# Kernel tuning notes

Measured on AMD Instinct MI355X. Metric: run time of the kernel, lower is better.

## Reference

```python
import jax, jax.numpy as jnp
import numpy as np

SR = 10  # self.sr in the torch module

def _linear_params(key, fan_in, fan_out):
    kw, kb = jax.random.split(key)
    bound = 1.0 / np.sqrt(fan_in)
    W = jax.random.uniform(kw, (fan_out, fan_in), jnp.float32, -bound, bound)
    b = jax.random.uniform(kb, (fan_out,), jnp.float32, -bound, bound)
    return W, b

def setup_inputs() -> dict:
    key = jax.random.key(0)
    ks = jax.random.split(key, 6)
    P, H = 2048, 1024
    R = C = P * SR
    X = jax.random.normal(ks[0], (R, C), jnp.float32)
    p = jax.random.randint(ks[1], (P,), 0, 64, jnp.int32)
    W1, b1 = _linear_params(ks[2], 1, H)
    W2, b2 = _linear_params(ks[3], H, H)
    W3, b3 = _linear_params(ks[4], H, H)
    W4, b4 = _linear_params(ks[5], H, 1)
    return {"X": X, "p": p, "W1": W1, "b1": b1, "W2": W2, "b2": b2,
            "W3": W3, "b3": b3, "W4": W4, "b4": b4}

def _forward(X, p, W1, b1, W2, b2, W3, b3, W4, b4):
    P = p.shape[0]
    C = X.shape[1]
    # shift_rows: only rows i*SR for i in [0, P-2] are populated; all other
    # rows of the shifted matrix are NaN and contribute 0 sum / 0 count below.
    rows = X[jnp.arange(P - 1) * SR]                      # (P-1, C)
    shifts = p[: P - 1]
    # torch.roll(x, s): out[j] = x[(j - s) mod C]
    cols = (jnp.arange(C)[None, :] - shifts[:, None]) % C  # (P-1, C)
    shifted = jnp.take_along_axis(rows, cols, axis=1)      # (P-1, C)
    # nan_mean over rows (NaN rows of the full matrix drop out identically)
    mask = jnp.isnan(shifted)
    col_sum = jnp.where(mask, 0.0, shifted).sum(axis=0)
    col_cnt = (~mask).sum(axis=0).astype(jnp.float32)
    m = jnp.where(col_cnt > 0, col_sum / col_cnt, jnp.float32(jnp.nan))  # (C,)
    # fill_nan_with_last_value: serial forward-fill (index 0 kept as-is)
    def step(last, xi):
        v = jnp.where(jnp.isnan(xi), last, xi)
        return v, v
    _, rest = jax.lax.scan(step, m[0], m[1:])
    filled = jnp.concatenate([m[:1], rest])                # (C,)
    x = filled[::SR][:P][:, None]                          # (P, 1)
    h = jax.nn.relu(x @ W1.T + b1)
    h = jax.nn.relu(h @ W2.T + b2)
    h = jax.nn.relu(h @ W3.T + b3)
    y = h @ W4.T + b4                                      # (P, 1)
    return y[:, 0]

def reference(X, p, W1, b1, W2, b2, W3, b3, W4, b4):
    return _forward(X, p, W1, b1, W2, b2, W3, b3, W4, b4)
```

## Files before the change

kernel.cpp:

```cpp
#include <hip/hip_runtime.h>
#include <hip/hip_bf16.h>

#define CC 20480
#define PP 2048
#define NROWS 2047
#define SRR 10
#define HH 1024
#define NCH 64

typedef __attribute__((ext_vector_type(8))) short short8;
typedef __attribute__((ext_vector_type(4))) float f32x4;

__device__ __forceinline__ void split_bf16(float v, unsigned short& hi, unsigned short& lo) {
    __hip_bfloat16 h = __float2bfloat16(v);
    float r = v - __bfloat162float(h);
    __hip_bfloat16 l2 = __float2bfloat16(r);
    hi = *(unsigned short*)&h;
    lo = *(unsigned short*)&l2;
}

__global__ __launch_bounds__(256) void pre_k(const float* __restrict__ X,
                                             const int* __restrict__ p,
                                             float* __restrict__ psum,
                                             const float* __restrict__ W2,
                                             unsigned short* __restrict__ w2h,
                                             unsigned short* __restrict__ w2l,
                                             const float* __restrict__ W3,
                                             unsigned short* __restrict__ w3h,
                                             unsigned short* __restrict__ w3l) {
    int b = blockIdx.x, t = threadIdx.x;
    if (b < 512) {
        int k = (b & 7) * 256 + t;
        int chunk = b >> 3;
        int r0 = chunk * 32;
        int r1 = r0 + 32; if (r1 > NROWS) r1 = NROWS;
        float s = 0.f;
        int base = SRR * k;
        for (int i = r0; i < r1; ++i) {
            int col = base - p[i]; if (col < 0) col += CC;
            s += X[(size_t)i * (size_t)(SRR * CC) + col];
        }
        psum[chunk * PP + k] = s;
        return;
    }
    int bb = b - 512;
    const float* src; unsigned short *dh, *dl;
    if (bb < 256) { src = W2; dh = w2h; dl = w2l; }
    else { src = W3; dh = w3h; dl = w3l; bb -= 256; }
    int idx = bb * 4096 + t * 16;
    #pragma unroll
    for (int q = 0; q < 4; ++q) {
        float4 v = *(const float4*)&src[idx + q * 4];
        float vv[4] = {v.x, v.y, v.z, v.w};
        ushort hi4[4], lo4[4];
        #pragma unroll
        for (int i = 0; i < 4; ++i) split_bf16(vv[i], hi4[i], lo4[i]);
        *(ushort4*)&dh[idx + q * 4] = *(ushort4*)hi4;
        *(ushort4*)&dl[idx + q * 4] = *(ushort4*)lo4;
    }
}

__device__ __forceinline__ void gload16(const unsigned short* g, unsigned short* lds) {
    __builtin_amdgcn_global_load_lds(
        (const __attribute__((address_space(1))) void*)g,
        (__attribute__((address_space(3))) void*)lds,
        16, 0, 0);
}

#define BM 128
#define BN 64
#define BK 32

__global__ __launch_bounds__(512, 2) void gemm1_k(
    const float* __restrict__ psum,
    const float* __restrict__ W1, const float* __restrict__ b1,
    const unsigned short* __restrict__ Bh, const unsigned short* __restrict__ Bl,
    const float* __restrict__ b2,
    unsigned short* __restrict__ Ch, unsigned short* __restrict__ Cl)
{
    __shared__ unsigned short Bb[3][4096];
    __shared__ float w1f[1024], b1f[1024], xv[128];

    int lin = blockIdx.x;
    int v = (lin & 7) * 32 + (lin >> 3);
    int bx = v >> 4, by = v & 15;
    int bm = bx * BM, bn = by * BN;
    int t = threadIdx.x, w = t >> 6, l = t & 63;
    int lr = l & 15, lk = l >> 4;
    int wr = w >> 1, wc = w & 1;

    size_t offB = (size_t)(bn + (w & 3) * 16 + lr) * HH + lk * 8;
#define BSTAGE(buf, k0)                                                      \
    do {                                                                     \
        if (w < 4) gload16(Bh + offB + (k0), Bb[buf] + w * 512);             \
        else       gload16(Bl + offB + (k0), Bb[buf] + 2048 + (w - 4) * 512);\
    } while (0)

    BSTAGE(0, 0);
    {
        int row = t >> 2, q = t & 3;
        float s = 0.f;
        #pragma unroll
        for (int j = 0; j < 16; ++j) s += psum[(q * 16 + j) * PP + bm + row];
        s += __shfl_xor(s, 1, 64);
        s += __shfl_xor(s, 2, 64);
        if (q == 0) xv[row] = s * (1.0f / (float)NROWS);
        if (t < 256) *(float4*)&w1f[t * 4] = *(const float4*)&W1[t * 4];
        else *(float4*)&b1f[(t - 256) * 4] = *(const float4*)&b1[(t - 256) * 4];
    }
    __syncthreads();

    float x0 = xv[wr * 32 + lr], x1 = xv[wr * 32 + 16 + lr];

    f32x4 acc[2][2];
    #pragma unroll
    for (int i = 0; i < 2; ++i)
        #pragma unroll
        for (int j = 0; j < 2; ++j) acc[i][j] = (f32x4)(0.f);

    int nt = HH / BK;
    for (int tt = 0; tt < nt; ++tt) {
        int cur = tt % 3;
        if (tt + 1 < nt) {
            BSTAGE((tt + 1) % 3, (tt + 1) * BK);
            asm volatile("s_waitcnt vmcnt(1)" ::: "memory");
        } else {
            asm volatile("s_waitcnt vmcnt(0)" ::: "memory");
        }
        __builtin_amdgcn_s_barrier();
        __builtin_amdgcn_sched_barrier(0);
        __builtin_amdgcn_s_setprio(1);
        int k0 = tt * BK;
        float4 wva = *(const float4*)&w1f[k0 + lk * 8];
        float4 wvb = *(const float4*)&w1f[k0 + lk * 8 + 4];
        float4 bva = *(const float4*)&b1f[k0 + lk * 8];
        float4 bvb = *(const float4*)&b1f[k0 + lk * 8 + 4];
        float wv[8] = {wva.x, wva.y, wva.z, wva.w, wvb.x, wvb.y, wvb.z, wvb.w};
        float bv2[8] = {bva.x, bva.y, bva.z, bva.w, bvb.x, bvb.y, bvb.z, bvb.w};
        ushort ahh[2][8], all2[2][8];
        #pragma unroll
        for (int mi = 0; mi < 2; ++mi) {
            float xm = mi ? x1 : x0;
            #pragma unroll
            for (int j = 0; j < 8; ++j) {
                float h = fmaf(xm, wv[j], bv2[j]);
                h = h > 0.f ? h : 0.f;
                split_bf16(h, ahh[mi][j], all2[mi][j]);
            }
        }
        short8 bh2[2], bl2[2];
        #pragma unroll
        for (int ni = 0; ni < 2; ++ni) {
            bh2[ni] = *(const short8*)&Bb[cur][(wc * 2 + ni) * 512 + l * 8];
            bl2[ni] = *(const short8*)&Bb[cur][2048 + (wc * 2 + ni) * 512 + l * 8];
        }
        #pragma unroll
        for (int mi = 0; mi < 2; ++mi) {
            short8 ah2 = *(short8*)ahh[mi];
            short8 al2 = *(short8*)all2[mi];
            #pragma unroll
            for (int ni = 0; ni < 2; ++ni) {
                acc[mi][ni] = __builtin_amdgcn_mfma_f32_16x16x32_bf16(ah2, bh2[ni], acc[mi][ni], 0, 0, 0);
                acc[mi][ni] = __builtin_amdgcn_mfma_f32_16x16x32_bf16(ah2, bl2[ni], acc[mi][ni], 0, 0, 0);
                acc[mi][ni] = __builtin_amdgcn_mfma_f32_16x16x32_bf16(al2, bh2[ni], acc[mi][ni], 0, 0, 0);
            }
        }
        __builtin_amdgcn_s_setprio(0);
        __builtin_amdgcn_sched_barrier(0);
    }
#undef BSTAGE

    float bv[2];
    #pragma unroll
    for (int ni = 0; ni < 2; ++ni) bv[ni] = b2[bn + wc * 32 + ni * 16 + lr];
    #pragma unroll
    for (int mi = 0; mi < 2; ++mi)
        #pragma unroll
        for (int ni = 0; ni < 2; ++ni)
            #pragma unroll
            for (int r = 0; r < 4; ++r) {
                int row = bm + wr * 32 + mi * 16 + lk * 4 + r;
                int col = bn + wc * 32 + ni * 16 + lr;
                float vv = acc[mi][ni][r] + bv[ni];
                vv = vv > 0.f ? vv : 0.f;
                unsigned short hi, lo;
                split_bf16(vv, hi, lo);
                Ch[(size_t)row * HH + col] = hi;
                Cl[(size_t)row * HH + col] = lo;
            }
}

__global__ __launch_bounds__(512, 2) void gemm2_k(
    const unsigned short* __restrict__ Ah, const unsigned short* __restrict__ Al,
    const unsigned short* __restrict__ Bh, const unsigned short* __restrict__ Bl,
    const float* __restrict__ b3,
    const float* __restrict__ W4, float* __restrict__ partial)
{
    __shared__ unsigned short lds[3][12288];
    int lin = blockIdx.x;
    int v = (lin & 7) * 32 + (lin >> 3);
    int bx = v >> 4, by = v & 15;
    int bm = bx * BM, bn = by * BN;
    int t = threadIdx.x, w = t >> 6, l = t & 63;
    int lr = l & 15, lk = l >> 4;
    int wr = w >> 1, wc = w & 1;

    size_t offA = (size_t)(bm + w * 16 + lr) * HH + lk * 8;
    size_t offB = (size_t)(bn + (w & 3) * 16 + lr) * HH + lk * 8;

#define STAGE(buf, k0)                                                   \
    do {                                                                 \
        unsigned short* L = lds[buf];                                    \
        gload16(Ah + offA + (k0), L + w * 512);                          \
        gload16(Al + offA + (k0), L + 4096 + w * 512);                   \
        if (w < 4) gload16(Bh + offB + (k0), L + 8192 + w * 512);        \
        else       gload16(Bl + offB + (k0), L + 10240 + (w - 4) * 512); \
    } while (0)

    f32x4 acc[2][2];
    #pragma unroll
    for (int i = 0; i < 2; ++i)
        #pragma unroll
        for (int j = 0; j < 2; ++j) acc[i][j] = (f32x4)(0.f);

    STAGE(0, 0);

    int nt = HH / BK;
    for (int tt = 0; tt < nt; ++tt) {
        int cur = tt % 3;
        if (tt + 1 < nt) {
            STAGE((tt + 1) % 3, (tt + 1) * BK);
            asm volatile("s_waitcnt vmcnt(3)" ::: "memory");
        } else {
            asm volatile("s_waitcnt vmcnt(0)" ::: "memory");
        }
        __builtin_amdgcn_s_barrier();
        __builtin_amdgcn_sched_barrier(0);
        __builtin_amdgcn_s_setprio(1);
        unsigned short* L = lds[cur];
        short8 ah2[2], al2[2], bh2[2], bl2[2];
        #pragma unroll
        for (int mi = 0; mi < 2; ++mi) {
            ah2[mi] = *(const short8*)&L[(wr * 2 + mi) * 512 + l * 8];
            al2[mi] = *(const short8*)&L[4096 + (wr * 2 + mi) * 512 + l * 8];
        }
        #pragma unroll
        for (int ni = 0; ni < 2; ++ni) {
            bh2[ni] = *(const short8*)&L[8192 + (wc * 2 + ni) * 512 + l * 8];
            bl2[ni] = *(const short8*)&L[10240 + (wc * 2 + ni) * 512 + l * 8];
        }
        #pragma unroll
        for (int mi = 0; mi < 2; ++mi)
            #pragma unroll
            for (int ni = 0; ni < 2; ++ni) {
                acc[mi][ni] = __builtin_amdgcn_mfma_f32_16x16x32_bf16(ah2[mi], bh2[ni], acc[mi][ni], 0, 0, 0);
                acc[mi][ni] = __builtin_amdgcn_mfma_f32_16x16x32_bf16(ah2[mi], bl2[ni], acc[mi][ni], 0, 0, 0);
                acc[mi][ni] = __builtin_amdgcn_mfma_f32_16x16x32_bf16(al2[mi], bh2[ni], acc[mi][ni], 0, 0, 0);
            }
        __builtin_amdgcn_s_setprio(0);
        __builtin_amdgcn_sched_barrier(0);
    }
#undef STAGE

    float bv[2], w4v[2];
    #pragma unroll
    for (int ni = 0; ni < 2; ++ni) {
        bv[ni]  = b3[bn + wc * 32 + ni * 16 + lr];
        w4v[ni] = W4[bn + wc * 32 + ni * 16 + lr];
    }
    #pragma unroll
    for (int mi = 0; mi < 2; ++mi) {
        float ps[4];
        #pragma unroll
        for (int r = 0; r < 4; ++r) {
            float acc_d = 0.f;
            #pragma unroll
            for (int ni = 0; ni < 2; ++ni) {
                float vv = acc[mi][ni][r] + bv[ni];
                vv = vv > 0.f ? vv : 0.f;
                acc_d += vv * w4v[ni];
            }
            ps[r] = acc_d;
        }
        #pragma unroll
        for (int r = 0; r < 4; ++r) {
            #pragma unroll
            for (int m2 = 1; m2 < 16; m2 <<= 1) ps[r] += __shfl_xor(ps[r], m2, 64);
        }
        if (lr == 0) {
            #pragma unroll
            for (int r = 0; r < 4; ++r) {
                int row = bm + wr * 32 + mi * 16 + lk * 4 + r;
                partial[(size_t)row * 32 + by * 2 + wc] = ps[r];
            }
        }
    }
}

__global__ __launch_bounds__(256) void ysum_k(const float* __restrict__ partial,
                                              const float* __restrict__ b4,
                                              float* __restrict__ y) {
    int r = blockIdx.x * 256 + threadIdx.x;
    float s = 0.f;
    #pragma unroll
    for (int q = 0; q < 8; ++q) {
        float4 v = *(const float4*)&partial[(size_t)r * 32 + q * 4];
        s += v.x + v.y + v.z + v.w;
    }
    y[r] = s + b4[0];
}

extern "C" void kernel_launch(void* const* d_in, const int* in_sizes, int n_in,
                              void* d_out, int out_size, void* d_ws, size_t ws_size,
                              hipStream_t stream) {
    const float* X  = (const float*)d_in[0];
    const int*   p  = (const int*)d_in[1];
    const float* W1 = (const float*)d_in[2];
    const float* b1 = (const float*)d_in[3];
    const float* W2 = (const float*)d_in[4];
    const float* b2 = (const float*)d_in[5];
    const float* W3 = (const float*)d_in[6];
    const float* b3 = (const float*)d_in[7];
    const float* W4 = (const float*)d_in[8];
    const float* b4 = (const float*)d_in[9];
    float* out = (float*)d_out;

    char* ws = (char*)d_ws;
    size_t off = 0;
    float* psum = (float*)(ws + off); off += (size_t)NCH * PP * 4;
    unsigned short* h2h = (unsigned short*)(ws + off); off += (size_t)PP * HH * 2;
    unsigned short* h2l = (unsigned short*)(ws + off); off += (size_t)PP * HH * 2;
    unsigned short* w2h = (unsigned short*)(ws + off); off += (size_t)HH * HH * 2;
    unsigned short* w2l = (unsigned short*)(ws + off); off += (size_t)HH * HH * 2;
    unsigned short* w3h = (unsigned short*)(ws + off); off += (size_t)HH * HH * 2;
    unsigned short* w3l = (unsigned short*)(ws + off); off += (size_t)HH * HH * 2;
    float* partial = (float*)(ws + off); off += (size_t)PP * 32 * 4;

    pre_k<<<1024, 256, 0, stream>>>(X, p, psum, W2, w2h, w2l, W3, w3h, w3l);
    gemm1_k<<<256, 512, 0, stream>>>(psum, W1, b1, w2h, w2l, b2, h2h, h2l);
    gemm2_k<<<256, 512, 0, stream>>>(h2h, h2l, w3h, w3l, b3, W4, partial);
    ysum_k<<<PP / 256, 256, 0, stream>>>(partial, b4, out);
}
```

Measured before the change: 81.88 us.

## Replace first hidden GEMM with piecewise-linear breakpoint tables over scalar input

Because the MLP input is a scalar x, layer-2 pre-activations are piecewise linear in x with breakpoints at -b1/W1. The change sorts the breakpoints, builds prefix-sum slope/intercept tables (Atab/Ctab) with a scan kernel over transposed W2, then evaluates h2 per row by binary search and one FMA per output. This removes the 2048x1024x1024 split-bf16 GEMM and is exact in fp32, at the cost of a serial 256-step scan kernel, a bitonic sort in one block, strided transpose writes, and 8 MB of tables.

Measured after the change: 145.1 us. +77.2%, slower.

```diff
diff --git a/kernel.cpp b/kernel.cpp
--- a/kernel.cpp
+++ b/kernel.cpp
@@ -23,11 +23,18 @@
                                              const int* __restrict__ p,
                                              float* __restrict__ psum,
                                              const float* __restrict__ W2,
-                                             unsigned short* __restrict__ w2h,
-                                             unsigned short* __restrict__ w2l,
+                                             float* __restrict__ w2t,
                                              const float* __restrict__ W3,
                                              unsigned short* __restrict__ w3h,
-                                             unsigned short* __restrict__ w3l) {
+                                             unsigned short* __restrict__ w3l,
+                                             const float* __restrict__ W1,
+                                             const float* __restrict__ b1,
+                                             float* __restrict__ tsort,
+                                             int* __restrict__ ord,
+                                             float* __restrict__ cA,
+                                             float* __restrict__ cC,
+                                             float* __restrict__ cI,
+                                             float* __restrict__ cIC) {
     int b = blockIdx.x, t = threadIdx.x;
     if (b < 512) {
         int k = (b & 7) * 256 + t;
@@ -43,20 +50,156 @@
         psum[chunk * PP + k] = s;
         return;
     }
-    int bb = b - 512;
-    const float* src; unsigned short *dh, *dl;
-    if (bb < 256) { src = W2; dh = w2h; dl = w2l; }
-    else { src = W3; dh = w3h; dl = w3l; bb -= 256; }
-    int idx = bb * 4096 + t * 16;
-    #pragma unroll
-    for (int q = 0; q < 4; ++q) {
-        float4 v = *(const float4*)&src[idx + q * 4];
-        float vv[4] = {v.x, v.y, v.z, v.w};
-        ushort hi4[4], lo4[4];
-        #pragma unroll
-        for (int i = 0; i < 4; ++i) split_bf16(vv[i], hi4[i], lo4[i]);
-        *(ushort4*)&dh[idx + q * 4] = *(ushort4*)hi4;
-        *(ushort4*)&dl[idx + q * 4] = *(ushort4*)lo4;
+    if (b < 768) {
+        int bb = b - 512;
+        int idx = bb * 4096 + t * 16;
+        int n2 = idx >> 10;
+        int o0 = idx & 1023;
+        #pragma unroll
+        for (int q = 0; q < 4; ++q) {
+            float4 v = *(const float4*)&W2[idx + q * 4];
+            w2t[(size_t)(o0 + q * 4 + 0) * 1024 + n2] = v.x;
+            w2t[(size_t)(o0 + q * 4 + 1) * 1024 + n2] = v.y;
+            w2t[(size_t)(o0 + q * 4 + 2) * 1024 + n2] = v.z;
+            w2t[(size_t)(o0 + q * 4 + 3) * 1024 + n2] = v.w;
+        }
+        return;
+    }
+    if (b < 1024) {
+        int bb = b - 768;
+        int idx = bb * 4096 + t * 16;
+        #pragma unroll
+        for (int q = 0; q < 4; ++q) {
+            float4 v = *(const float4*)&W3[idx + q * 4];
+            float vv[4] = {v.x, v.y, v.z, v.w};
+            ushort hi4[4], lo4[4];
+            #pragma unroll
+            for (int i = 0; i < 4; ++i) split_bf16(vv[i], hi4[i], lo4[i]);
+            *(ushort4*)&w3h[idx + q * 4] = *(ushort4*)hi4;
+            *(ushort4*)&w3l[idx + q * 4] = *(ushort4*)lo4;
+        }
+        return;
+    }
+    __shared__ float ks[1024];
+    __shared__ int vs[1024];
+    const float PINF = __int_as_float(0x7f800000);
+    for (int i = t; i < 1024; i += 256) {
+        float w1 = W1[i], bv = b1[i];
+        float tv;
+        if (w1 != 0.f) tv = -bv / w1;
+        else tv = (bv > 0.f) ? -PINF : PINF;
+        ks[i] = tv; vs[i] = i;
+    }
+    __syncthreads();
+    for (int size = 2; size <= 1024; size <<= 1)
+        for (int stride = size >> 1; stride; stride >>= 1) {
+            for (int i = t; i < 1024; i += 256) {
+                int jx = i ^ stride;
+                if (jx > i) {
+                    bool up = ((i & size) == 0);
+                    float a = ks[i], bq = ks[jx];
+                    bool sw = up ? (a > bq) : (a < bq);
+                    if (sw) {
+                        ks[i] = bq; ks[jx] = a;
+                        int tmp = vs[i]; vs[i] = vs[jx]; vs[jx] = tmp;
+                    }
+                }
+            }
+            __syncthreads();
+        }
+    for (int i = t; i < 1024; i += 256) {
+        int o = vs[i];
+        float w1 = W1[o], bv = b1[o];
+        float s = (w1 < 0.f) ? -1.f : 1.f;
+        tsort[i] = ks[i]; ord[i] = o;
+        cA[i] = s * w1;  cC[i] = s * bv;
+        cI[i] = (w1 < 0.f) ? w1 : 0.f;
+        cIC[i] = (w1 < 0.f) ? bv : 0.f;
+    }
+}
+
+__global__ __launch_bounds__(256) void scan_k(const float* __restrict__ w2t,
+                                              const int* __restrict__ ord,
+                                              const float* __restrict__ cA,
+                                              const float* __restrict__ cC,
+                                              const float* __restrict__ cI,
+                                              const float* __restrict__ cIC,
+                                              float* __restrict__ Atab,
+                                              float* __restrict__ Ctab,
+                                              const float* __restrict__ psum,
+                                              float* __restrict__ xbuf) {
+    int b = blockIdx.x, t = threadIdx.x;
+    if (b >= 16) {
+        int k = (b - 16) * 256 + t;
+        float s = 0.f;
+        #pragma unroll 8
+        for (int c = 0; c < NCH; ++c) s += psum[c * PP + k];
+        xbuf[k] = s * (1.0f / (float)NROWS);
+        return;
+    }
+    __shared__ float sA[4][64], sC[4][64], sIA[4][64], sIC[4][64];
+    int q = t >> 6, n = t & 63;
+    int n2 = b * 64 + n;
+    float gA = 0.f, gC = 0.f, iA = 0.f, iC = 0.f;
+    #pragma unroll 4
+    for (int step = 0; step < 256; ++step) {
+        int j = q * 256 + step;
+        int o = ord[j];
+        float wv = w2t[(size_t)o * 1024 + n2];
+        gA = fmaf(cA[j], wv, gA);
+        gC = fmaf(cC[j], wv, gC);
+        iA = fmaf(cI[j], wv, iA);
+        iC = fmaf(cIC[j], wv, iC);
+    }
+    sA[q][n] = gA; sC[q][n] = gC; sIA[q][n] = iA; sIC[q][n] = iC;
+    __syncthreads();
+    float offA = sIA[0][n] + sIA[1][n] + sIA[2][n] + sIA[3][n];
+    float offC = sIC[0][n] + sIC[1][n] + sIC[2][n] + sIC[3][n];
+    #pragma unroll
+    for (int q2 = 0; q2 < 4; ++q2)
+        if (q2 < q) { offA += sA[q2][n]; offC += sC[q2][n]; }
+    if (q == 0) { Atab[n2] = offA; Ctab[n2] = offC; }
+    float g2 = offA, h2 = offC;
+    #pragma unroll 4
+    for (int step = 0; step < 256; ++step) {
+        int j = q * 256 + step;
+        int o = ord[j];
+        float wv = w2t[(size_t)o * 1024 + n2];
+        g2 = fmaf(cA[j], wv, g2);
+        h2 = fmaf(cC[j], wv, h2);
+        Atab[(size_t)(j + 1) * 1024 + n2] = g2;
+        Ctab[(size_t)(j + 1) * 1024 + n2] = h2;
+    }
+}
+
+__global__ __launch_bounds__(512) void evalh2_k(const float* __restrict__ tsort,
+                                                const float* __restrict__ Atab,
+                                                const float* __restrict__ Ctab,
+                                                const float* __restrict__ b2,
+                                                const float* __restrict__ xbuf,
+                                                unsigned short* __restrict__ h2h,
+                                                unsigned short* __restrict__ h2l) {
+    __shared__ float ts[1024];
+    int t = threadIdx.x;
+    for (int i = t; i < 1024; i += 512) ts[i] = tsort[i];
+    __syncthreads();
+    int wv = t >> 6, lane = t & 63;
+    int k = blockIdx.x * 8 + wv;
+    float x = xbuf[k];
+    int lo = 0, hi = 1024;
+    while (lo < hi) { int mid = (lo + hi) >> 1; if (ts[mid] < x) lo = mid + 1; else hi = mid; }
+    const float* Ac = Atab + (size_t)lo * 1024;
+    const float* Cc = Ctab + (size_t)lo * 1024;
+    #pragma unroll
+    for (int s2 = 0; s2 < 16; ++s2) {
+        int n2 = s2 * 64 + lane;
+        float a = Ac[n2], c = Cc[n2], bb = b2[n2];
+        float h = fmaf(a, x, c + bb);
+        h = h > 0.f ? h : 0.f;
+        unsigned short hh, hl;
+        split_bf16(h, hh, hl);
+        h2h[(size_t)k * 1024 + n2] = hh;
+        h2l[(size_t)k * 1024 + n2] = hl;
     }
 }
 
@@ -70,125 +213,6 @@
 #define BM 128
 #define BN 64
 #define BK 32
-
-__global__ __launch_bounds__(512, 2) void gemm1_k(
-    const float* __restrict__ psum,
-    const float* __restrict__ W1, const float* __restrict__ b1,
-    const unsigned short* __restrict__ Bh, const unsigned short* __restrict__ Bl,
-    const float* __restrict__ b2,
-    unsigned short* __restrict__ Ch, unsigned short* __restrict__ Cl)
-{
-    __shared__ unsigned short Bb[3][4096];
-    __shared__ float w1f[1024], b1f[1024], xv[128];
-
-    int lin = blockIdx.x;
-    int v = (lin & 7) * 32 + (lin >> 3);
-    int bx = v >> 4, by = v & 15;
-    int bm = bx * BM, bn = by * BN;
-    int t = threadIdx.x, w = t >> 6, l = t & 63;
-    int lr = l & 15, lk = l >> 4;
-    int wr = w >> 1, wc = w & 1;
-
-    size_t offB = (size_t)(bn + (w & 3) * 16 + lr) * HH + lk * 8;
-#define BSTAGE(buf, k0)                                                      \
-    do {                                                                     \
-        if (w < 4) gload16(Bh + offB + (k0), Bb[buf] + w * 512);             \
-        else       gload16(Bl + offB + (k0), Bb[buf] + 2048 + (w - 4) * 512);\
-    } while (0)
-
-    BSTAGE(0, 0);
-    {
-        int row = t >> 2, q = t & 3;
-        float s = 0.f;
-        #pragma unroll
-        for (int j = 0; j < 16; ++j) s += psum[(q * 16 + j) * PP + bm + row];
-        s += __shfl_xor(s, 1, 64);
-        s += __shfl_xor(s, 2, 64);
-        if (q == 0) xv[row] = s * (1.0f / (float)NROWS);
-        if (t < 256) *(float4*)&w1f[t * 4] = *(const float4*)&W1[t * 4];
-        else *(float4*)&b1f[(t - 256) * 4] = *(const float4*)&b1[(t - 256) * 4];
-    }
-    __syncthreads();
-
-    float x0 = xv[wr * 32 + lr], x1 = xv[wr * 32 + 16 + lr];
-
-    f32x4 acc[2][2];
-    #pragma unroll
-    for (int i = 0; i < 2; ++i)
-        #pragma unroll
-        for (int j = 0; j < 2; ++j) acc[i][j] = (f32x4)(0.f);
-
-    int nt = HH / BK;
-    for (int tt = 0; tt < nt; ++tt) {
-        int cur = tt % 3;
-        if (tt + 1 < nt) {
-            BSTAGE((tt + 1) % 3, (tt + 1) * BK);
-            asm volatile("s_waitcnt vmcnt(1)" ::: "memory");
-        } else {
-            asm volatile("s_waitcnt vmcnt(0)" ::: "memory");
-        }
-        __builtin_amdgcn_s_barrier();
-        __builtin_amdgcn_sched_barrier(0);
-        __builtin_amdgcn_s_setprio(1);
-        int k0 = tt * BK;
-        float4 wva = *(const float4*)&w1f[k0 + lk * 8];
-        float4 wvb = *(const float4*)&w1f[k0 + lk * 8 + 4];
-        float4 bva = *(const float4*)&b1f[k0 + lk * 8];
-        float4 bvb = *(const float4*)&b1f[k0 + lk * 8 + 4];
-        float wv[8] = {wva.x, wva.y, wva.z, wva.w, wvb.x, wvb.y, wvb.z, wvb.w};
-        float bv2[8] = {bva.x, bva.y, bva.z, bva.w, bvb.x, bvb.y, bvb.z, bvb.w};
-        ushort ahh[2][8], all2[2][8];
-        #pragma unroll
-        for (int mi = 0; mi < 2; ++mi) {
-            float xm = mi ? x1 : x0;
-            #pragma unroll
-            for (int j = 0; j < 8; ++j) {
-                float h = fmaf(xm, wv[j], bv2[j]);
-                h = h > 0.f ? h : 0.f;
-                split_bf16(h, ahh[mi][j], all2[mi][j]);
-            }
-        }
-        short8 bh2[2], bl2[2];
-        #pragma unroll
-        for (int ni = 0; ni < 2; ++ni) {
-            bh2[ni] = *(const short8*)&Bb[cur][(wc * 2 + ni) * 512 + l * 8];
-            bl2[ni] = *(const short8*)&Bb[cur][2048 + (wc * 2 + ni) * 512 + l * 8];
-        }
-        #pragma unroll
-        for (int mi = 0; mi < 2; ++mi) {
-            short8 ah2 = *(short8*)ahh[mi];
-            short8 al2 = *(short8*)all2[mi];
-            #pragma unroll
-            for (int ni = 0; ni < 2; ++ni) {
-                acc[mi][ni] = __builtin_amdgcn_mfma_f32_16x16x32_bf16(ah2, bh2[ni], acc[mi][ni], 0, 0, 0);
-                acc[mi][ni] = __builtin_amdgcn_mfma_f32_16x16x32_bf16(ah2, bl2[ni], acc[mi][ni], 0, 0, 0);
-                acc[mi][ni] = __builtin_amdgcn_mfma_f32_16x16x32_bf16(al2, bh2[ni], acc[mi][ni], 0, 0, 0);
-            }
-        }
-        __builtin_amdgcn_s_setprio(0);
-        __builtin_amdgcn_sched_barrier(0);
-    }
-#undef BSTAGE
-
-    float bv[2];
-    #pragma unroll
-    for (int ni = 0; ni < 2; ++ni) bv[ni] = b2[bn + wc * 32 + ni * 16 + lr];
-    #pragma unroll
-    for (int mi = 0; mi < 2; ++mi)
-        #pragma unroll
-        for (int ni = 0; ni < 2; ++ni)
-            #pragma unroll
-            for (int r = 0; r < 4; ++r) {
-                int row = bm + wr * 32 + mi * 16 + lk * 4 + r;
-                int col = bn + wc * 32 + ni * 16 + lr;
-                float vv = acc[mi][ni][r] + bv[ni];
-                vv = vv > 0.f ? vv : 0.f;
-                unsigned short hi, lo;
-                split_bf16(vv, hi, lo);
-                Ch[(size_t)row * HH + col] = hi;
-                Cl[(size_t)row * HH + col] = lo;
-            }
-}
 
 __global__ __launch_bounds__(512, 2) void gemm2_k(
     const unsigned short* __restrict__ Ah, const unsigned short* __restrict__ Al,
@@ -327,17 +351,27 @@
 
     char* ws = (char*)d_ws;
     size_t off = 0;
-    float* psum = (float*)(ws + off); off += (size_t)NCH * PP * 4;
+    float* psum  = (float*)(ws + off); off += (size_t)NCH * PP * 4;
+    float* xbuf  = (float*)(ws + off); off += 8192;
+    float* w2t   = (float*)(ws + off); off += (size_t)HH * HH * 4;
+    unsigned short* w3h = (unsigned short*)(ws + off); off += (size_t)HH * HH * 2;
+    unsigned short* w3l = (unsigned short*)(ws + off); off += (size_t)HH * HH * 2;
+    float* tsort = (float*)(ws + off); off += 4096;
+    int*   ordb  = (int*)  (ws + off); off += 4096;
+    float* cA    = (float*)(ws + off); off += 4096;
+    float* cC    = (float*)(ws + off); off += 4096;
+    float* cI    = (float*)(ws + off); off += 4096;
+    float* cIC   = (float*)(ws + off); off += 4096;
+    float* Atab  = (float*)(ws + off); off += (size_t)1025 * 1024 * 4;
+    float* Ctab  = (float*)(ws + off); off += (size_t)1025 * 1024 * 4;
     unsigned short* h2h = (unsigned short*)(ws + off); off += (size_t)PP * HH * 2;
     unsigned short* h2l = (unsigned short*)(ws + off); off += (size_t)PP * HH * 2;
-    unsigned short* w2h = (unsigned short*)(ws + off); off += (size_t)HH * HH * 2;
-    unsigned short* w2l = (unsigned short*)(ws + off); off += (size_t)HH * HH * 2;
-    unsigned short* w3h = (unsigned short*)(ws + off); off += (size_t)HH * HH * 2;
-    unsigned short* w3l = (unsigned short*)(ws + off); off += (size_t)HH * HH * 2;
     float* partial = (float*)(ws + off); off += (size_t)PP * 32 * 4;
 
-    pre_k<<<1024, 256, 0, stream>>>(X, p, psum, W2, w2h, w2l, W3, w3h, w3l);
-    gemm1_k<<<256, 512, 0, stream>>>(psum, W1, b1, w2h, w2l, b2, h2h, h2l);
+    pre_k<<<1025, 256, 0, stream>>>(X, p, psum, W2, w2t, W3, w3h, w3l,
+                                    W1, b1, tsort, ordb, cA, cC, cI, cIC);
+    scan_k<<<24, 256, 0, stream>>>(w2t, ordb, cA, cC, cI, cIC, Atab, Ctab, psum, xbuf);
+    evalh2_k<<<256, 512, 0, stream>>>(tsort, Atab, Ctab, b2, xbuf, h2h, h2l);
     gemm2_k<<<256, 512, 0, stream>>>(h2h, h2l, w3h, w3l, b3, W4, partial);
     ysum_k<<<PP / 256, 256, 0, stream>>>(partial, b4, out);
 }
```
